# Optimization experiments

Hardware: AMD Instinct MI355X
Metric: run time of the kernel (lower is better)

## Reference

```python
import jax, jax.numpy as jnp
import numpy as np


def cross_scan(x):
    # x: (B, D, H, W) -> xs: (B, 8, D, L)  (row, col, rev-row, rev-col, diag, antidiag, rev-diag, rev-antidiag)
    B, D, H, W = x.shape
    L = H * W
    hs = jnp.arange(H)[:, None]
    ws = jnp.arange(W)[None, :]
    x0 = x.reshape(B, D, L)                          # row-major
    x1 = jnp.swapaxes(x, 2, 3).reshape(B, D, L)      # column-major
    gd = x[:, :, hs, (hs + ws) % W]                  # diagonal gather (B,D,H,W)
    ga = x[:, :, hs, (ws - hs) % W]                  # antidiagonal gather
    x4 = jnp.swapaxes(gd, -1, -2).reshape(B, D, L)
    x5 = jnp.swapaxes(ga, -1, -2).reshape(B, D, L)
    return jnp.stack([x0, x1, x0[..., ::-1], x1[..., ::-1],
                      x4, x5, x4[..., ::-1], x5[..., ::-1]], axis=1)


def cross_merge(ys, H, W):
    # ys: (B, 8, D, L) -> (B, D, L), inverse-scatter + sum of all 8 directions
    B, K, D, L = ys.shape
    hs = jnp.arange(H)[:, None]
    ws = jnp.arange(W)[None, :]
    y = ys[:, 0] + ys[:, 2, :, ::-1]
    yt = (ys[:, 1] + ys[:, 3, :, ::-1]).reshape(B, D, W, H)
    y = y + jnp.swapaxes(yt, -1, -2).reshape(B, D, L)
    # diagonal scatter: result[h, w'] = t[h, (w'-h) % W]
    td = jnp.swapaxes((ys[:, 4] + ys[:, 6, :, ::-1]).reshape(B, D, W, H), -1, -2)
    y = y + td[:, :, hs, (ws - hs) % W].reshape(B, D, L)
    # antidiagonal scatter: result[h, w'] = t[h, (w'+h) % W]
    ta = jnp.swapaxes((ys[:, 5] + ys[:, 7, :, ::-1]).reshape(B, D, W, H), -1, -2)
    y = y + ta[:, :, hs, (ws + hs) % W].reshape(B, D, L)
    return y


def selective_scan(u, delta, A, Bs, Cs, Ds):
    # u, delta: (B, KD, L); A: (KD, N); Bs, Cs: (B, K, N, L); Ds: (KD,)
    Bb, KD, L = u.shape
    K = Bs.shape[1]
    Dh = KD // K
    N = A.shape[1]
    u_ = jnp.moveaxis(u.reshape(Bb, K, Dh, L), -1, 0)        # (L,B,K,Dh)
    d_ = jnp.moveaxis(delta.reshape(Bb, K, Dh, L), -1, 0)
    B_ = jnp.moveaxis(Bs, -1, 0)                              # (L,B,K,N)
    C_ = jnp.moveaxis(Cs, -1, 0)
    A_ = A.reshape(K, Dh, N)

    def step(h, inp):
        u_t, d_t, b_t, c_t = inp
        dA = jnp.exp(d_t[..., None] * A_)                     # (B,K,Dh,N)
        h = h * dA + (d_t * u_t)[..., None] * b_t[:, :, None, :]
        y = jnp.einsum('bkdn,bkn->bkd', h, c_t)
        return h, y

    h0 = jnp.zeros((Bb, K, Dh, N), u.dtype)
    _, ys = jax.lax.scan(step, h0, (u_, d_, B_, C_))          # ys: (L,B,K,Dh)
    ys = jnp.moveaxis(ys, 0, -1).reshape(Bb, KD, L)
    return ys + u * Ds[None, :, None]


def setup_inputs() -> dict:
    key = jax.random.key(0)
    ks = jax.random.split(key, 6)
    B, D, H, W = 2, 192, 64, 64
    K, N, R = 8, 16, 6
    x = jax.random.normal(ks[0], (B, D, H, W), jnp.float32)
    x_proj_weight = jax.random.normal(ks[1], (K, R + 2 * N, D), jnp.float32) * (1.0 / np.sqrt(D))
    dt_projs_weight = jax.random.normal(ks[2], (K, D, R), jnp.float32) * (0.1 / np.sqrt(R))
    dt_projs_bias = jax.random.normal(ks[3], (K, D), jnp.float32) * 0.1
    A_logs = jax.random.uniform(ks[4], (K * D, N), jnp.float32)
    Ds = jax.random.normal(ks[5], (K * D,), jnp.float32)
    ln_w = jnp.ones((D,), jnp.float32)
    ln_b = jnp.zeros((D,), jnp.float32)
    return {"x": x, "x_proj_weight": x_proj_weight, "dt_projs_weight": dt_projs_weight,
            "dt_projs_bias": dt_projs_bias, "A_logs": A_logs, "Ds": Ds,
            "ln_w": ln_w, "ln_b": ln_b}


def reference(x, x_proj_weight, dt_projs_weight, dt_projs_bias, A_logs, Ds, ln_w, ln_b):
    B, D, H, W = x.shape
    K = x_proj_weight.shape[0]
    N = A_logs.shape[1]
    R = dt_projs_weight.shape[2]
    L = H * W
    xs = cross_scan(x)                                            # (B,K,D,L)
    x_dbl = jnp.einsum('bkdl,kcd->bkcl', xs, x_proj_weight)       # (B,K,R+2N,L)
    dts, Bs, Cs = jnp.split(x_dbl, [R, R + N], axis=2)
    dts = jnp.einsum('bkrl,kdr->bkdl', dts, dt_projs_weight)      # (B,K,D,L)
    u = xs.reshape(B, K * D, L)
    delta = jax.nn.softplus(dts.reshape(B, K * D, L) + dt_projs_bias.reshape(1, K * D, 1))
    A = -jnp.exp(A_logs)                                          # (KD,N)
    ys = selective_scan(u, delta, A, Bs, Cs, Ds)                  # (B,KD,L)
    y = cross_merge(ys.reshape(B, K, D, L), H, W)                 # (B,D,L)
    y = jnp.swapaxes(y, 1, 2)                                     # (B,L,D)
    mu = y.mean(-1, keepdims=True)
    var = y.var(-1, keepdims=True)
    y = (y - mu) / jnp.sqrt(var + 1e-5) * ln_w + ln_b             # out_norm (LayerNorm)
    return y.reshape(B, H, W, D)
```

## Files before the change

### kernel.cpp

```cpp
#include <hip/hip_runtime.h>
#include <math.h>

#define BB   2
#define DD   192
#define LL   4096
#define KK   8
#define NN   16
#define RR   6
#define C38  38
#define CPAD 40
#define PQS  17
#define NCH  64
#define CLEN (LL / NCH)

__device__ __forceinline__ float fexp2(float x) { return __builtin_amdgcn_exp2f(x); }
__device__ __forceinline__ float flog2(float x) { return __builtin_amdgcn_logf(x); }

__device__ __forceinline__ float softplus_f(float x) {
  return fmaxf(x, 0.f) + 0.69314718f * flog2(1.f + fexp2(-1.44269504f * fabsf(x)));
}

__device__ __forceinline__ int src_index(int k, int l) {
  int ll = (k & 2) ? (LL - 1 - l) : l;
  int kb = k & 5;
  if (kb == 0) return ll;
  int h = ll & 63, w = ll >> 6;
  if (kb == 1) return (h << 6) + w;
  if (kb == 4) return (h << 6) + ((h + w) & 63);
  return (h << 6) + ((w - h) & 63);
}

__global__ __launch_bounds__(256) void transpose_x(const float* __restrict__ x,
                                                   float* __restrict__ xT) {
  __shared__ float tile[32][33];
  int b  = blockIdx.z;
  int p0 = blockIdx.x * 32;
  int d0 = blockIdx.y * 32;
  int tx = threadIdx.x, ty = threadIdx.y;
  #pragma unroll
  for (int i = 0; i < 32; i += 8)
    tile[ty + i][tx] = x[((size_t)(b * DD + d0 + ty + i)) * LL + p0 + tx];
  __syncthreads();
  #pragma unroll
  for (int i = 0; i < 32; i += 8)
    xT[((size_t)(b * LL + p0 + ty + i)) * DD + d0 + tx] = tile[tx][ty + i];
}

__global__ __launch_bounds__(256) void proj_kernel(const float* __restrict__ xT,
                                                   const float* __restrict__ W,
                                                   float* __restrict__ xdbl) {
  int k = blockIdx.y, b = blockIdx.z;
  int tx = threadIdx.x;
  int lloc = tx & 127, half = tx >> 7;
  int l = blockIdx.x * 128 + lloc;
  __shared__ __align__(16) float sm[DD * CPAD];
  for (int i = tx; i < C38 * DD; i += 256) {
    int c = i / DD, dq = i - c * DD;
    sm[dq * CPAD + c] = W[(k * C38 + c) * DD + dq];
  }
  for (int dq = tx; dq < DD; dq += 256) { sm[dq * CPAD + 38] = 0.f; sm[dq * CPAD + 39] = 0.f; }
  __syncthreads();

  int p = src_index(k, l);
  const float4* xrow4 = (const float4*)(xT + ((size_t)b * LL + p) * DD) + half * 24;
  const float* wbase = sm + half * 96 * CPAD;
  float4 acc[10];
  #pragma unroll
  for (int c = 0; c < 10; ++c) acc[c] = make_float4(0.f, 0.f, 0.f, 0.f);

  for (int d4 = 0; d4 < 24; ++d4) {
    float4 xv = xrow4[d4];
    #pragma unroll
    for (int s = 0; s < 4; ++s) {
      float xs = (s == 0) ? xv.x : (s == 1) ? xv.y : (s == 2) ? xv.z : xv.w;
      const float4* w4 = (const float4*)(wbase + (d4 * 4 + s) * CPAD);
      #pragma unroll
      for (int c = 0; c < 10; ++c) {
        float4 wv = w4[c];
        acc[c].x = fmaf(wv.x, xs, acc[c].x);
        acc[c].y = fmaf(wv.y, xs, acc[c].y);
        acc[c].z = fmaf(wv.z, xs, acc[c].z);
        acc[c].w = fmaf(wv.w, xs, acc[c].w);
      }
    }
  }
  __syncthreads();
  if (half == 1) {
    float* pr = sm + lloc * 41;
    const float* af = (const float*)acc;
    #pragma unroll
    for (int c = 0; c < 38; ++c) pr[c] = af[c];
  }
  __syncthreads();
  if (half == 0) {
    const float* pr = sm + lloc * 41;
    float* af = (float*)acc;
    #pragma unroll
    for (int c = 0; c < 38; ++c) af[c] += pr[c];
    float* orow = xdbl + ((size_t)((b * KK + k) * LL) + l) * CPAD;
    float4* o4 = (float4*)orow;
    #pragma unroll
    for (int c = 0; c < 9; ++c) o4[c] = acc[c];
    orow[36] = acc[9].x;
    orow[37] = acc[9].y;
  }
}

template <bool FINAL>
__global__ __launch_bounds__(384, 5) void scan_kernel(
    const float* __restrict__ xT, const float* __restrict__ xdbl,
    const float* __restrict__ A_logs, const float* __restrict__ dtw,
    const float* __restrict__ dtb, const float* __restrict__ Ds,
    float* __restrict__ Pq, float* __restrict__ Y) {
  const int lane = threadIdx.x;
  const int ng   = lane >> 5;
  const int dd   = threadIdx.y;
  const int bk   = blockIdx.x;
  const int chunk = blockIdx.y;
  const int b = bk >> 3, k = bk & 7;
  const int d  = dd * 32 + (lane & 31);
  const int kd = k * DD + d;
  const int ch = bk * DD + d;

  float An2[8];
  {
    const float* ap = A_logs + (size_t)kd * NN + ng * 8;
    #pragma unroll
    for (int j = 0; j < 8; ++j) An2[j] = -__expf(ap[j]) * 1.44269504f;
  }
  float wdt[RR];
  #pragma unroll
  for (int r = 0; r < RR; ++r) wdt[r] = dtw[kd * RR + r];
  const float bias = dtb[kd];
  const float dval = FINAL ? Ds[kd] : 0.f;

  float h[8];
  if constexpr (FINAL) {
    const float* h0p = Pq + ((size_t)ch * NCH + chunk) * PQS + 1 + ng * 8;
    #pragma unroll
    for (int j = 0; j < 8; ++j) h[j] = h0p[j];
  } else {
    #pragma unroll
    for (int j = 0; j < 8; ++j) h[j] = 0.f;
  }

  const int l0 = chunk * CLEN;
  const float* rowbase = xdbl + ((size_t)(bk * LL) + l0) * CPAD;
  const float* xTb = xT + (size_t)b * LL * DD + d;

  float S = 0.f;
  float sp[2], uu[2], Bv[2][8], Cv[2][8];
  int   pp[2];

  auto LOADT = [&](int t, int s) {
    const float* row = rowbase + (size_t)t * CPAD;
    const float2* r2 = (const float2*)row;
    float2 d01 = r2[0], d23 = r2[1], d45 = r2[2];
    float dts = bias;
    dts = fmaf(d01.x, wdt[0], dts);
    dts = fmaf(d01.y, wdt[1], dts);
    dts = fmaf(d23.x, wdt[2], dts);
    dts = fmaf(d23.y, wdt[3], dts);
    dts = fmaf(d45.x, wdt[4], dts);
    dts = fmaf(d45.y, wdt[5], dts);
    sp[s] = softplus_f(dts);
    const float2* bq = (const float2*)(row + 6 + ng * 8);
    #pragma unroll
    for (int j = 0; j < 4; ++j) {
      float2 v = bq[j];
      Bv[s][2 * j] = v.x; Bv[s][2 * j + 1] = v.y;
    }
    if constexpr (FINAL) {
      const float2* cq = (const float2*)(row + 22 + ng * 8);
      #pragma unroll
      for (int j = 0; j < 4; ++j) {
        float2 v = cq[j];
        Cv[s][2 * j] = v.x; Cv[s][2 * j + 1] = v.y;
      }
    }
    int p = src_index(k, l0 + t);
    pp[s] = p;
    uu[s] = xTb[(size_t)p * DD];
  };

  auto COMPUTE = [&](int s) {
    float spv = sp[s];
    float du = spv * uu[s];
    #pragma unroll
    for (int j = 0; j < 8; ++j) {
      float e = fexp2(spv * An2[j]);
      h[j] = fmaf(h[j], e, du * Bv[s][j]);
    }
    if constexpr (FINAL) {
      float y = 0.f;
      #pragma unroll
      for (int j = 0; j < 8; ++j) y = fmaf(h[j], Cv[s][j], y);
      y += __shfl_xor(y, 32, 64);
      if (ng == 0) {
        float outv = fmaf(uu[s], dval, y);
        atomicAdd(&Y[(size_t)(b * LL + pp[s]) * DD + d], outv);
      }
    } else {
      S += spv;
    }
  };

  LOADT(0, 0);
  for (int t = 0; t < CLEN; t += 2) {
    LOADT(t + 1, 1);
    COMPUTE(0);
    int t2 = (t + 2 < CLEN) ? t + 2 : CLEN - 1;
    LOADT(t2, 0);
    COMPUTE(1);
  }

  if constexpr (!FINAL) {
    float* rec = Pq + ((size_t)ch * NCH + chunk) * PQS;
    if (ng == 0) rec[0] = S;
    float* qp = rec + 1 + ng * 8;
    #pragma unroll
    for (int j = 0; j < 8; ++j) qp[j] = h[j];
  }
}

__global__ __launch_bounds__(256) void stitch_kernel(float* __restrict__ Pq,
                                                     const float* __restrict__ A_logs) {
  int lane = threadIdx.x & 63;
  int gw = (blockIdx.x * 256 + threadIdx.x) >> 6;
  int ch = gw >> 4, n = gw & 15;
  int kd = ch % (KK * DD);
  float An2 = -__expf(A_logs[(size_t)kd * NN + n]) * 1.44269504f;

  float* rec = Pq + ((size_t)ch * NCH + lane) * PQS;
  float P = fexp2(An2 * rec[0]);
  float q = rec[1 + n];

  float Pt = P, qt = q;
  #pragma unroll
  for (int off = 1; off < 64; off <<= 1) {
    float Pp = __shfl_up(Pt, off, 64);
    float qp = __shfl_up(qt, off, 64);
    if (lane >= off) { qt = fmaf(Pt, qp, qt); Pt *= Pp; }
  }
  float hx = __shfl_up(qt, 1, 64);
  if (lane == 0) hx = 0.f;
  rec[1 + n] = hx;
}

__global__ __launch_bounds__(256) void ln_kernel(const float* __restrict__ Y,
                                                 const float* __restrict__ lw,
                                                 const float* __restrict__ lb,
                                                 float* __restrict__ out) {
  int lane = threadIdx.x & 63;
  int row = blockIdx.x * 4 + (threadIdx.x >> 6);
  const float* yr = Y + (size_t)row * DD;
  float v0 = yr[lane], v1 = yr[lane + 64], v2 = yr[lane + 128];
  float s1 = v0 + v1 + v2;
  float s2 = v0 * v0 + v1 * v1 + v2 * v2;
  #pragma unroll
  for (int m = 32; m >= 1; m >>= 1) {
    s1 += __shfl_xor(s1, m, 64);
    s2 += __shfl_xor(s2, m, 64);
  }
  float mu = s1 * (1.f / DD);
  float var = s2 * (1.f / DD) - mu * mu;
  float inv = rsqrtf(var + 1e-5f);
  float* orow = out + (size_t)row * DD;
  orow[lane]       = (v0 - mu) * inv * lw[lane]       + lb[lane];
  orow[lane + 64]  = (v1 - mu) * inv * lw[lane + 64]  + lb[lane + 64];
  orow[lane + 128] = (v2 - mu) * inv * lw[lane + 128] + lb[lane + 128];
}

extern "C" void kernel_launch(void* const* d_in, const int* in_sizes, int n_in,
                              void* d_out, int out_size, void* d_ws, size_t ws_size,
                              hipStream_t stream) {
  const float* x      = (const float*)d_in[0];
  const float* xpw    = (const float*)d_in[1];
  const float* dtw    = (const float*)d_in[2];
  const float* dtb    = (const float*)d_in[3];
  const float* A_logs = (const float*)d_in[4];
  const float* Ds     = (const float*)d_in[5];
  const float* ln_w   = (const float*)d_in[6];
  const float* ln_b   = (const float*)d_in[7];
  float* out = (float*)d_out;

  float* ws   = (float*)d_ws;
  float* xT   = ws;
  float* xdbl = xT + 1572864;
  float* Y    = xdbl + 2621440;
  float* Pq   = Y + 1572864;

  hipMemsetAsync(Y, 0, 1572864 * sizeof(float), stream);
  transpose_x<<<dim3(LL / 32, DD / 32, BB), dim3(32, 8), 0, stream>>>(x, xT);
  proj_kernel<<<dim3(LL / 128, KK, BB), 256, 0, stream>>>(xT, xpw, xdbl);
  scan_kernel<false><<<dim3(BB * KK, NCH), dim3(64, 6), 0, stream>>>(
      xT, xdbl, A_logs, dtw, dtb, Ds, Pq, Y);
  stitch_kernel<<<(3072 * 16 * 64) / 256, 256, 0, stream>>>(Pq, A_logs);
  scan_kernel<true><<<dim3(BB * KK, NCH), dim3(64, 6), 0, stream>>>(
      xT, xdbl, A_logs, dtw, dtb, Ds, Pq, Y);
  ln_kernel<<<(BB * LL) / 4, 256, 0, stream>>>(Y, ln_w, ln_b, out);
}
```

Before: 250.2 us.

## Stage scan chunk rows in LDS, relayout carry arrays, deepen u prefetch

The scan kernel now copies its chunk's projected rows (dt, B and, in the final pass, C) cooperatively into shared memory, padded so B and C can be read as float4. This replaces per-thread redundant global row loads. The chunk carry records move from an interleaved per-channel record of 17 floats to separate S and Q arrays laid out chunk-major, so the per-channel writes and reads are coalesced. The u gathers are software-pipelined four steps ahead instead of one, and the occupancy hint drops from 5 to 4 blocks to make room for the extra registers and shared memory.

```diff
diff --git a/kernel.cpp b/kernel.cpp
--- a/kernel.cpp
+++ b/kernel.cpp
@@ -9,9 +9,9 @@
 #define RR   6
 #define C38  38
 #define CPAD 40
-#define PQS  17
 #define NCH  64
 #define CLEN (LL / NCH)
+#define NCHAN (BB * KK * DD)
 
 __device__ __forceinline__ float fexp2(float x) { return __builtin_amdgcn_exp2f(x); }
 __device__ __forceinline__ float flog2(float x) { return __builtin_amdgcn_logf(x); }
@@ -107,20 +107,37 @@
 }
 
 template <bool FINAL>
-__global__ __launch_bounds__(384, 5) void scan_kernel(
+__global__ __launch_bounds__(384, 4) void scan_kernel(
     const float* __restrict__ xT, const float* __restrict__ xdbl,
     const float* __restrict__ A_logs, const float* __restrict__ dtw,
     const float* __restrict__ dtb, const float* __restrict__ Ds,
-    float* __restrict__ Pq, float* __restrict__ Y) {
-  const int lane = threadIdx.x;
-  const int ng   = lane >> 5;
-  const int dd   = threadIdx.y;
-  const int bk   = blockIdx.x;
+    float* __restrict__ Sarr, float* __restrict__ Qarr, float* __restrict__ Y) {
+  constexpr int ROWF  = FINAL ? 40 : 24;
+  constexpr int ROWF2 = ROWF / 2;
+  constexpr int SRCF2 = FINAL ? 19 : 11;
+
+  __shared__ __align__(16) float rows[CLEN * ROWF];
+
+  const int lane  = threadIdx.x;
+  const int ng    = lane >> 5;
+  const int dd    = threadIdx.y;
+  const int tid   = dd * 64 + lane;
+  const int bk    = blockIdx.x;
   const int chunk = blockIdx.y;
   const int b = bk >> 3, k = bk & 7;
   const int d  = dd * 32 + (lane & 31);
   const int kd = k * DD + d;
   const int ch = bk * DD + d;
+  const int l0 = chunk * CLEN;
+
+  {
+    const float2* src2 = (const float2*)(xdbl + ((size_t)(bk * LL) + l0) * CPAD);
+    float2* dst2 = (float2*)rows;
+    for (int i = tid; i < CLEN * SRCF2; i += 384) {
+      int r = i / SRCF2, c = i - r * SRCF2;
+      dst2[r * ROWF2 + c + (c >= 3)] = src2[r * (CPAD / 2) + c];
+    }
+  }
 
   float An2[8];
   {
@@ -136,7 +153,7 @@
 
   float h[8];
   if constexpr (FINAL) {
-    const float* h0p = Pq + ((size_t)ch * NCH + chunk) * PQS + 1 + ng * 8;
+    const float* h0p = Qarr + ((size_t)chunk * NCHAN + ch) * NN + ng * 8;
     #pragma unroll
     for (int j = 0; j < 8; ++j) h[j] = h0p[j];
   } else {
@@ -144,96 +161,90 @@
     for (int j = 0; j < 8; ++j) h[j] = 0.f;
   }
 
-  const int l0 = chunk * CLEN;
-  const float* rowbase = xdbl + ((size_t)(bk * LL) + l0) * CPAD;
   const float* xTb = xT + (size_t)b * LL * DD + d;
-
   float S = 0.f;
-  float sp[2], uu[2], Bv[2][8], Cv[2][8];
-  int   pp[2];
-
-  auto LOADT = [&](int t, int s) {
-    const float* row = rowbase + (size_t)t * CPAD;
-    const float2* r2 = (const float2*)row;
-    float2 d01 = r2[0], d23 = r2[1], d45 = r2[2];
+
+  __syncthreads();
+
+  auto STEP = [&](int t, int p, float u) {
+    const float* row = rows + t * ROWF;
     float dts = bias;
-    dts = fmaf(d01.x, wdt[0], dts);
-    dts = fmaf(d01.y, wdt[1], dts);
-    dts = fmaf(d23.x, wdt[2], dts);
-    dts = fmaf(d23.y, wdt[3], dts);
-    dts = fmaf(d45.x, wdt[4], dts);
-    dts = fmaf(d45.y, wdt[5], dts);
-    sp[s] = softplus_f(dts);
-    const float2* bq = (const float2*)(row + 6 + ng * 8);
-    #pragma unroll
-    for (int j = 0; j < 4; ++j) {
-      float2 v = bq[j];
-      Bv[s][2 * j] = v.x; Bv[s][2 * j + 1] = v.y;
-    }
-    if constexpr (FINAL) {
-      const float2* cq = (const float2*)(row + 22 + ng * 8);
-      #pragma unroll
-      for (int j = 0; j < 4; ++j) {
-        float2 v = cq[j];
-        Cv[s][2 * j] = v.x; Cv[s][2 * j + 1] = v.y;
-      }
-    }
-    int p = src_index(k, l0 + t);
-    pp[s] = p;
-    uu[s] = xTb[(size_t)p * DD];
-  };
-
-  auto COMPUTE = [&](int s) {
-    float spv = sp[s];
-    float du = spv * uu[s];
+    dts = fmaf(row[0], wdt[0], dts);
+    dts = fmaf(row[1], wdt[1], dts);
+    dts = fmaf(row[2], wdt[2], dts);
+    dts = fmaf(row[3], wdt[3], dts);
+    dts = fmaf(row[4], wdt[4], dts);
+    dts = fmaf(row[5], wdt[5], dts);
+    float spv = softplus_f(dts);
+    float du = spv * u;
+    const float4* bq = (const float4*)(row + 8 + ng * 8);
+    float4 b0 = bq[0], b1 = bq[1];
+    float Bvv[8] = {b0.x, b0.y, b0.z, b0.w, b1.x, b1.y, b1.z, b1.w};
     #pragma unroll
     for (int j = 0; j < 8; ++j) {
       float e = fexp2(spv * An2[j]);
-      h[j] = fmaf(h[j], e, du * Bv[s][j]);
+      h[j] = fmaf(h[j], e, du * Bvv[j]);
     }
     if constexpr (FINAL) {
+      const float4* cq = (const float4*)(row + 24 + ng * 8);
+      float4 c0 = cq[0], c1 = cq[1];
+      float Cvv[8] = {c0.x, c0.y, c0.z, c0.w, c1.x, c1.y, c1.z, c1.w};
       float y = 0.f;
       #pragma unroll
-      for (int j = 0; j < 8; ++j) y = fmaf(h[j], Cv[s][j], y);
+      for (int j = 0; j < 8; ++j) y = fmaf(h[j], Cvv[j], y);
       y += __shfl_xor(y, 32, 64);
       if (ng == 0) {
-        float outv = fmaf(uu[s], dval, y);
-        atomicAdd(&Y[(size_t)(b * LL + pp[s]) * DD + d], outv);
+        atomicAdd(&Y[(size_t)(b * LL + p) * DD + d], fmaf(u, dval, y));
       }
     } else {
       S += spv;
     }
   };
 
-  LOADT(0, 0);
-  for (int t = 0; t < CLEN; t += 2) {
-    LOADT(t + 1, 1);
-    COMPUTE(0);
-    int t2 = (t + 2 < CLEN) ? t + 2 : CLEN - 1;
-    LOADT(t2, 0);
-    COMPUTE(1);
+  int ppA[4], ppB[4];
+  float uuA[4], uuB[4];
+  #pragma unroll
+  for (int s = 0; s < 4; ++s) {
+    int p = src_index(k, l0 + s);
+    ppA[s] = p; uuA[s] = xTb[(size_t)p * DD];
+  }
+  for (int tb = 0; tb < CLEN; tb += 8) {
+    #pragma unroll
+    for (int s = 0; s < 4; ++s) {
+      int p = src_index(k, l0 + tb + 4 + s);
+      ppB[s] = p; uuB[s] = xTb[(size_t)p * DD];
+    }
+    #pragma unroll
+    for (int s = 0; s < 4; ++s) STEP(tb + s, ppA[s], uuA[s]);
+    int nb = (tb + 8 < CLEN) ? tb + 8 : 0;
+    #pragma unroll
+    for (int s = 0; s < 4; ++s) {
+      int p = src_index(k, l0 + nb + s);
+      ppA[s] = p; uuA[s] = xTb[(size_t)p * DD];
+    }
+    #pragma unroll
+    for (int s = 0; s < 4; ++s) STEP(tb + 4 + s, ppB[s], uuB[s]);
   }
 
   if constexpr (!FINAL) {
-    float* rec = Pq + ((size_t)ch * NCH + chunk) * PQS;
-    if (ng == 0) rec[0] = S;
-    float* qp = rec + 1 + ng * 8;
+    if (ng == 0) Sarr[(size_t)chunk * NCHAN + ch] = S;
+    float* qp = Qarr + ((size_t)chunk * NCHAN + ch) * NN + ng * 8;
     #pragma unroll
     for (int j = 0; j < 8; ++j) qp[j] = h[j];
   }
 }
 
-__global__ __launch_bounds__(256) void stitch_kernel(float* __restrict__ Pq,
+__global__ __launch_bounds__(256) void stitch_kernel(float* __restrict__ Sarr,
+                                                     float* __restrict__ Qarr,
                                                      const float* __restrict__ A_logs) {
   int lane = threadIdx.x & 63;
   int gw = (blockIdx.x * 256 + threadIdx.x) >> 6;
-  int ch = gw >> 4, n = gw & 15;
-  int kd = ch % (KK * DD);
+  int chn = gw >> 4, n = gw & 15;
+  int kd = chn % (KK * DD);
   float An2 = -__expf(A_logs[(size_t)kd * NN + n]) * 1.44269504f;
 
-  float* rec = Pq + ((size_t)ch * NCH + lane) * PQS;
-  float P = fexp2(An2 * rec[0]);
-  float q = rec[1 + n];
+  float P = fexp2(An2 * Sarr[(size_t)lane * NCHAN + chn]);
+  float q = Qarr[((size_t)lane * NCHAN + chn) * NN + n];
 
   float Pt = P, qt = q;
   #pragma unroll
@@ -244,7 +255,7 @@
   }
   float hx = __shfl_up(qt, 1, 64);
   if (lane == 0) hx = 0.f;
-  rec[1 + n] = hx;
+  Qarr[((size_t)lane * NCHAN + chn) * NN + n] = hx;
 }
 
 __global__ __launch_bounds__(256) void ln_kernel(const float* __restrict__ Y,
@@ -288,15 +299,16 @@
   float* xT   = ws;
   float* xdbl = xT + 1572864;
   float* Y    = xdbl + 2621440;
-  float* Pq   = Y + 1572864;
+  float* Sarr = Y + 1572864;
+  float* Qarr = Sarr + 196608;
 
   hipMemsetAsync(Y, 0, 1572864 * sizeof(float), stream);
   transpose_x<<<dim3(LL / 32, DD / 32, BB), dim3(32, 8), 0, stream>>>(x, xT);
   proj_kernel<<<dim3(LL / 128, KK, BB), 256, 0, stream>>>(xT, xpw, xdbl);
   scan_kernel<false><<<dim3(BB * KK, NCH), dim3(64, 6), 0, stream>>>(
-      xT, xdbl, A_logs, dtw, dtb, Ds, Pq, Y);
-  stitch_kernel<<<(3072 * 16 * 64) / 256, 256, 0, stream>>>(Pq, A_logs);
+      xT, xdbl, A_logs, dtw, dtb, Ds, Sarr, Qarr, Y);
+  stitch_kernel<<<(NCHAN * 16 * 64) / 256, 256, 0, stream>>>(Sarr, Qarr, A_logs);
   scan_kernel<true><<<dim3(BB * KK, NCH), dim3(64, 6), 0, stream>>>(
-      xT, xdbl, A_logs, dtw, dtb, Ds, Pq, Y);
+      xT, xdbl, A_logs, dtw, dtb, Ds, Sarr, Qarr, Y);
   ln_kernel<<<(BB * LL) / 4, 256, 0, stream>>>(Y, ln_w, ln_b, out);
 }
```

Result: no change. 253.2 us (+1.2%).
